# Performance work log

Hardware: AMD Instinct MI355X
Metric: run time of the kernel (lower is better)

Reference implementation:

```python
import jax, jax.numpy as jnp
import numpy as np

B, H, W, C = 16, 128, 128, 128
Wh = Ww = 8
SH = 4  # shift size
NH = 4  # heads
HD = C // NH
N = Wh * Ww
HID = 4 * C
EPS = 1e-3  # keras LayerNormalization default epsilon
SCALE = HD ** -0.5


def _rel_pos_index():
    coords = np.stack(np.meshgrid(np.arange(Wh), np.arange(Ww), indexing='ij'))  # (2,Wh,Ww)
    flat = coords.reshape(2, -1)
    rel = flat[:, :, None] - flat[:, None, :]  # (2,N,N)
    rel = rel.transpose(1, 2, 0) + np.array([Wh - 1, Ww - 1])
    rel = rel * np.array([2 * Ww - 1, 1])
    return rel.sum(-1).astype(np.int32)  # (N,N)


def _attn_mask():
    img = np.zeros((1, H, W, 1))
    h_sl = (slice(0, H - Wh), slice(H - Wh, H - SH), slice(H - SH, H))
    w_sl = (slice(0, W - Ww), slice(W - Ww, W - SH), slice(W - SH, W))
    cnt = 0
    for hs in h_sl:
        for ws in w_sl:
            img[:, hs, ws, :] = cnt
            cnt += 1
    mw = img.reshape(1, H // Wh, Wh, W // Ww, Ww, 1).transpose(0, 1, 3, 2, 4, 5).reshape(-1, N)
    am = mw[:, None, :] - mw[:, :, None]
    return np.where(am != 0, -100.0, 0.0).astype(np.float32)  # (nW,N,N)


def setup_inputs() -> dict:
    key = jax.random.key(0)
    ks = jax.random.split(key, 12)
    s = 0.02
    return {
        'x': jax.random.normal(ks[0], (B, H * W, C), jnp.float32),
        'w_qkv': jax.random.normal(ks[1], (C, 3 * C), jnp.float32) * s,
        'b_qkv': jnp.zeros((3 * C,), jnp.float32),
        'bias_table': jax.random.normal(ks[2], ((2 * Wh - 1) * (2 * Ww - 1), NH), jnp.float32) * s,
        'w_proj': jax.random.normal(ks[3], (C, C), jnp.float32) * s,
        'b_proj': jnp.zeros((C,), jnp.float32),
        'g1': jnp.ones((C,), jnp.float32),
        'be1': jnp.zeros((C,), jnp.float32),
        'w_fc1': jax.random.normal(ks[4], (C, HID), jnp.float32) * s,
        'b_fc1': jnp.zeros((HID,), jnp.float32),
        'w_fc2': jax.random.normal(ks[5], (HID, C), jnp.float32) * s,
        'b_fc2': jnp.zeros((C,), jnp.float32),
        'g2': jnp.ones((C,), jnp.float32),
        'be2': jnp.zeros((C,), jnp.float32),
        'rel_index': jnp.asarray(_rel_pos_index()),
        'attn_mask': jnp.asarray(_attn_mask()),
    }


def _ln(x, g, b):
    m = jnp.mean(x, -1, keepdims=True)
    v = jnp.mean(jnp.square(x - m), -1, keepdims=True)
    return (x - m) * jax.lax.rsqrt(v + EPS) * g + b


def _block(x, w_qkv, b_qkv, bias_table, w_proj, b_proj, g1, be1,
           w_fc1, b_fc1, w_fc2, b_fc2, g2, be2, rel_index, attn_mask):
    xi = x.reshape(B, H, W, C)
    xs = jnp.roll(xi, (-SH, -SH), axis=(1, 2))
    # window partition -> (B*nW, N, C)
    xw = xs.reshape(B, H // Wh, Wh, W // Ww, Ww, C).transpose(0, 1, 3, 2, 4, 5).reshape(-1, N, C)
    qkv = (xw @ w_qkv + b_qkv).reshape(-1, N, 3, NH, HD).transpose(2, 0, 3, 1, 4)
    q, k, v = qkv[0] * SCALE, qkv[1], qkv[2]
    attn = jnp.einsum('bhnd,bhmd->bhnm', q, k)  # (B*nW, NH, N, N)
    rpb = bias_table[rel_index.reshape(-1)].reshape(N, N, NH).transpose(2, 0, 1)
    attn = attn + rpb[None]
    nW = attn_mask.shape[0]
    attn = attn.reshape(-1, nW, NH, N, N) + attn_mask[None, :, None]
    attn = jax.nn.softmax(attn.reshape(-1, NH, N, N), axis=-1)
    out = jnp.einsum('bhnm,bhmd->bhnd', attn, v).transpose(0, 2, 1, 3).reshape(-1, N, C)
    out = out @ w_proj + b_proj
    # window reverse + unshift
    out = out.reshape(B, H // Wh, W // Ww, Wh, Ww, C).transpose(0, 1, 3, 2, 4, 5).reshape(B, H, W, C)
    out = jnp.roll(out, (SH, SH), axis=(1, 2)).reshape(B, H * W, C)
    # NOTE: this module applies norm AFTER the sublayers (post-norm residual)
    x = x + _ln(out, g1, be1)
    h = jax.nn.gelu(x @ w_fc1 + b_fc1, approximate=False) @ w_fc2 + b_fc2
    x = x + _ln(h, g2, be2)
    return x


def reference(x, w_qkv, b_qkv, bias_table, w_proj, b_proj, g1, be1,
              w_fc1, b_fc1, w_fc2, b_fc2, g2, be2, rel_index, attn_mask):
    return _block(x, w_qkv, b_qkv, bias_table, w_proj, b_proj, g1, be1,
                  w_fc1, b_fc1, w_fc2, b_fc2, g2, be2, rel_index, attn_mask)
```

## Files before the change

kernel.cpp:

```cpp
#include <hip/hip_runtime.h>
#include <hip/hip_bf16.h>
#include <math.h>

typedef unsigned short u16;
typedef unsigned int   u32;

typedef __bf16 bf16x8 __attribute__((ext_vector_type(8)));
typedef float  f32x4  __attribute__((ext_vector_type(4)));
#define MFMA_B16 __builtin_amdgcn_mfma_f32_16x16x32_bf16

__device__ __forceinline__ u16 f2b(float f) {
    union { __bf16 h; u16 u; } v; v.h = (__bf16)f; return v.u;
}
__device__ __forceinline__ u32 pk2(float a, float b) {
    union { __bf16 h[2]; u32 u; } v;
    v.h[0] = (__bf16)a; v.h[1] = (__bf16)b; return v.u;
}
__device__ __forceinline__ bf16x8 pk8(float4 f0, float4 f1) {
    bf16x8 r;
    r[0] = (__bf16)f0.x; r[1] = (__bf16)f0.y; r[2] = (__bf16)f0.z; r[3] = (__bf16)f0.w;
    r[4] = (__bf16)f1.x; r[5] = (__bf16)f1.y; r[6] = (__bf16)f1.z; r[7] = (__bf16)f1.w;
    return r;
}

__device__ __forceinline__ float gelu_fast(float v) {
    const float z = v * (1.5957691f + 0.07135486f * v * v);
    return v * __builtin_amdgcn_rcpf(1.0f + __expf(-z));
}

__device__ __forceinline__ int qk_idx(int row, int d) {
    return row * 32 + (d ^ (((row >> 1) & 3) << 3));
}
__device__ __forceinline__ int p_idx(int row, int col) {
    return row * 64 + (col ^ ((row & 7) << 3));
}

#define SCALE_ 0.17677669529663687f
#define EPS_   1e-3f


__global__ __launch_bounds__(256) void swin_prep(
    const float* __restrict__ w_qkv, const float* __restrict__ w_proj,
    const float* __restrict__ w_fc1, const float* __restrict__ w_fc2,
    const float* __restrict__ bias_table, const int* __restrict__ rel_index,
    const float* __restrict__ attn_mask,
    u16* __restrict__ wqkvT, u16* __restrict__ wprojT,
    u16* __restrict__ w1T, u16* __restrict__ w2T, float* __restrict__ rpbm)
{
    const int idx = blockIdx.x * 256 + threadIdx.x;
    if (idx < 49152) {
        const int o = idx >> 7, c = idx & 127;
        wqkvT[idx] = f2b(w_qkv[c * 384 + o]);
    } else if (idx < 65536) {
        const int i2 = idx - 49152;
        const int o = i2 >> 7, c = i2 & 127;
        wprojT[i2] = f2b(w_proj[c * 128 + o]);
    } else if (idx < 131072) {
        const int i2 = idx - 65536;
        const int o = i2 >> 7, c = i2 & 127;
        w1T[i2] = f2b(w_fc1[c * 512 + o]);
    } else if (idx < 196608) {
        const int i2 = idx - 131072;
        const int o = i2 >> 9, u = i2 & 511;
        w2T[i2] = f2b(w_fc2[u * 128 + o]);
    } else if (idx < 262144) {
        const int i2 = idx - 196608;
        const int cls = i2 >> 14, rem = i2 & 16383;
        const int h = rem >> 12, ij = rem & 4095;
        const int widx = ((cls & 2) ? 240 : 0) + ((cls & 1) ? 15 : 0);
        rpbm[i2] = bias_table[rel_index[ij] * 4 + h] + attn_mask[widx * 4096 + ij];
    }
}

#define VA_OFF  16384
#define AO_OFF  0
#define X2F_OFF 4352

__global__ __launch_bounds__(256, 3) void swin_attn_mfma(
    const float* __restrict__ x, const u16* __restrict__ wqkvT, const float* __restrict__ b_qkv,
    const u16* __restrict__ wprojT, const float* __restrict__ b_proj,
    const float* __restrict__ g1, const float* __restrict__ be1,
    const float* __restrict__ rpbm, float* __restrict__ x1out)
{
    __shared__ __align__(16) u16 sm[25600];
    const int tid  = threadIdx.x;
    const int w    = tid >> 6;
    const int lane = tid & 63;
    const int l15  = lane & 15;
    const int quad = lane >> 4;
    const int win  = blockIdx.x;
    const int b = win >> 8, wr = (win >> 4) & 15, wc = win & 15;

    size_t rowb[4];
    #pragma unroll
    for (int mi = 0; mi < 4; mi++) {
        const int t  = mi * 16 + l15;
        const int hh = (wr * 8 + (t >> 3) + 4) & 127;
        const int ww = (wc * 8 + (t & 7) + 4) & 127;
        rowb[mi] = ((size_t)((b * 128 + hh) * 128 + ww)) * 128;
    }

    {
        f32x4 acc[6][4];
        #pragma unroll
        for (int n = 0; n < 6; n++) {
            const float bq = b_qkv[(n >> 1) * 128 + w * 32 + (n & 1) * 16 + l15];
            #pragma unroll
            for (int mi = 0; mi < 4; mi++) acc[n][mi] = (f32x4){bq, bq, bq, bq};
        }
        #pragma unroll
        for (int ks = 0; ks < 4; ks++) {
            bf16x8 a[4], bb[6];
            #pragma unroll
            for (int mi = 0; mi < 4; mi++) {
                const float4 f0 = *(const float4*)(x + rowb[mi] + ks * 32 + quad * 8);
                const float4 f1 = *(const float4*)(x + rowb[mi] + ks * 32 + quad * 8 + 4);
                a[mi] = pk8(f0, f1);
            }
            #pragma unroll
            for (int n = 0; n < 6; n++)
                bb[n] = *(const bf16x8*)(wqkvT
                    + (size_t)((n >> 1) * 128 + w * 32 + (n & 1) * 16 + l15) * 128 + ks * 32 + quad * 8);
            #pragma unroll
            for (int n = 0; n < 6; n++)
                #pragma unroll
                for (int mi = 0; mi < 4; mi++)
                    acc[n][mi] = MFMA_B16(a[mi], bb[n], acc[n][mi], 0, 0, 0);
        }
        #pragma unroll
        for (int n = 0; n < 6; n++) {
            const int s = n >> 1, d = (n & 1) * 16 + l15;
            #pragma unroll
            for (int mi = 0; mi < 4; mi++) {
                if (s < 2) {
                    const int base = w * 4096 + s * 2048;
                    const float sc = s ? 1.0f : SCALE_;
                    #pragma unroll
                    for (int r = 0; r < 4; r++) {
                        const int row = mi * 16 + quad * 4 + r;
                        sm[base + qk_idx(row, d)] = f2b(acc[n][mi][r] * sc);
                    }
                } else {
                    const int t0 = mi * 16 + quad * 4;
                    const u32 w0 = pk2(acc[n][mi][0], acc[n][mi][1]);
                    const u32 w1 = pk2(acc[n][mi][2], acc[n][mi][3]);
                    *(uint2*)(sm + VA_OFF + w * 2304 + d * 72 + t0) = make_uint2(w0, w1);
                }
            }
        }
    }

    float sinv[4][4];
    {
        const float* rb = rpbm + (size_t)((((wr == 15) ? 2 : 0) | ((wc == 15) ? 1 : 0)) * 4 + w) * 4096;
        f32x4 S[4][4];
        #pragma unroll
        for (int mi = 0; mi < 4; mi++)
            #pragma unroll
            for (int ni = 0; ni < 4; ni++)
                #pragma unroll
                for (int r = 0; r < 4; r++)
                    S[mi][ni][r] = rb[(mi * 16 + quad * 4 + r) * 64 + ni * 16 + l15];
        bf16x8 aq[4], bk[4];
        #pragma unroll
        for (int mi = 0; mi < 4; mi++)
            aq[mi] = *(const bf16x8*)(sm + w * 4096 + qk_idx(mi * 16 + l15, quad * 8));
        #pragma unroll
        for (int ni = 0; ni < 4; ni++)
            bk[ni] = *(const bf16x8*)(sm + w * 4096 + 2048 + qk_idx(ni * 16 + l15, quad * 8));
        #pragma unroll
        for (int mi = 0; mi < 4; mi++)
            #pragma unroll
            for (int ni = 0; ni < 4; ni++)
                S[mi][ni] = MFMA_B16(aq[mi], bk[ni], S[mi][ni], 0, 0, 0);
        #pragma unroll
        for (int mi = 0; mi < 4; mi++) {
            #pragma unroll
            for (int r = 0; r < 4; r++) {
                float m0 = fmaxf(fmaxf(S[mi][0][r], S[mi][1][r]), fmaxf(S[mi][2][r], S[mi][3][r]));
                m0 = fmaxf(m0, __shfl_xor(m0, 1));
                m0 = fmaxf(m0, __shfl_xor(m0, 2));
                m0 = fmaxf(m0, __shfl_xor(m0, 4));
                m0 = fmaxf(m0, __shfl_xor(m0, 8));
                float s0 = 0.0f;
                #pragma unroll
                for (int ni = 0; ni < 4; ni++) {
                    const float e = __expf(S[mi][ni][r] - m0);
                    S[mi][ni][r] = e;
                    s0 += e;
                }
                s0 += __shfl_xor(s0, 1);
                s0 += __shfl_xor(s0, 2);
                s0 += __shfl_xor(s0, 4);
                s0 += __shfl_xor(s0, 8);
                sinv[mi][r] = __builtin_amdgcn_rcpf(s0);
            }
        }

        #pragma unroll
        for (int mi = 0; mi < 4; mi++)
            #pragma unroll
            for (int ni = 0; ni < 4; ni++)
                #pragma unroll
                for (int r = 0; r < 4; r++)
                    sm[w * 4096 + p_idx(mi * 16 + quad * 4 + r, ni * 16 + l15)] = f2b(S[mi][ni][r]);

        f32x4 O[4][2];
        #pragma unroll
        for (int mi = 0; mi < 4; mi++)
            #pragma unroll
            for (int ni = 0; ni < 2; ni++) O[mi][ni] = (f32x4){0.f, 0.f, 0.f, 0.f};
        #pragma unroll
        for (int ks = 0; ks < 2; ks++) {
            bf16x8 ap[4], bv[2];
            #pragma unroll
            for (int mi = 0; mi < 4; mi++)
                ap[mi] = *(const bf16x8*)(sm + w * 4096 + p_idx(mi * 16 + l15, ks * 32 + quad * 8));
            #pragma unroll
            for (int ni = 0; ni < 2; ni++)
                bv[ni] = *(const bf16x8*)(sm + VA_OFF + w * 2304 + (ni * 16 + l15) * 72 + ks * 32 + quad * 8);
            #pragma unroll
            for (int mi = 0; mi < 4; mi++)
                #pragma unroll
                for (int ni = 0; ni < 2; ni++)
                    O[mi][ni] = MFMA_B16(ap[mi], bv[ni], O[mi][ni], 0, 0, 0);
        }
        __syncthreads();

        #pragma unroll
        for (int mi = 0; mi < 4; mi++)
            #pragma unroll
            for (int ni = 0; ni < 2; ni++)
                #pragma unroll
                for (int r = 0; r < 4; r++)
                    sm[AO_OFF + (mi * 16 + quad * 4 + r) * 136 + w * 32 + ni * 16 + l15]
                        = f2b(O[mi][ni][r] * sinv[mi][r]);
    }
    __syncthreads();

    float4 xres[8];
    size_t gout;
    {
        const int t = tid >> 2, part = tid & 3;
        const int hh = (wr * 8 + (t >> 3) + 4) & 127;
        const int ww = (wc * 8 + (t & 7) + 4) & 127;
        gout = ((size_t)((b * 128 + hh) * 128 + ww)) * 128 + part * 32;
        #pragma unroll
        for (int k = 0; k < 8; k++)
            xres[k] = *(const float4*)(x + gout + k * 4);
    }
    {
        f32x4 X2[4][2];
        #pragma unroll
        for (int ni = 0; ni < 2; ni++) {
            const float bp = b_proj[w * 32 + ni * 16 + l15];
            #pragma unroll
            for (int mi = 0; mi < 4; mi++) X2[mi][ni] = (f32x4){bp, bp, bp, bp};
        }
        #pragma unroll
        for (int ks = 0; ks < 4; ks++) {
            bf16x8 aa[4], bw[2];
            #pragma unroll
            for (int mi = 0; mi < 4; mi++)
                aa[mi] = *(const bf16x8*)(sm + AO_OFF + (mi * 16 + l15) * 136 + ks * 32 + quad * 8);
            #pragma unroll
            for (int ni = 0; ni < 2; ni++)
                bw[ni] = *(const bf16x8*)(wprojT + (size_t)(w * 32 + ni * 16 + l15) * 128 + ks * 32 + quad * 8);
            #pragma unroll
            for (int mi = 0; mi < 4; mi++)
                #pragma unroll
                for (int ni = 0; ni < 2; ni++)
                    X2[mi][ni] = MFMA_B16(aa[mi], bw[ni], X2[mi][ni], 0, 0, 0);
        }
        float* X2f = (float*)sm + X2F_OFF;
        #pragma unroll
        for (int mi = 0; mi < 4; mi++)
            #pragma unroll
            for (int ni = 0; ni < 2; ni++)
                #pragma unroll
                for (int r = 0; r < 4; r++)
                    X2f[(mi * 16 + quad * 4 + r) * 132 + w * 32 + ni * 16 + l15] = X2[mi][ni][r];
    }
    __syncthreads();

    {
        const int t = tid >> 2, part = tid & 3;
        const float* Xr = (const float*)sm + X2F_OFF + t * 132 + part * 32;
        float4 xr[8];
        float s1 = 0.f, s2 = 0.f;
        #pragma unroll
        for (int k = 0; k < 8; k++) {
            xr[k] = *(const float4*)(Xr + k * 4);
            s1 += xr[k].x + xr[k].y + xr[k].z + xr[k].w;
            s2 += xr[k].x * xr[k].x + xr[k].y * xr[k].y
                + xr[k].z * xr[k].z + xr[k].w * xr[k].w;
        }
        s1 += __shfl_xor(s1, 1); s1 += __shfl_xor(s1, 2);
        s2 += __shfl_xor(s2, 1); s2 += __shfl_xor(s2, 2);
        const float m  = s1 * 0.0078125f;
        const float vr = fmaxf(s2 * 0.0078125f - m * m, 0.f);
        const float rs = rsqrtf(vr + EPS_);
        #pragma unroll
        for (int k = 0; k < 8; k++) {
            const int c4 = k * 4;
            const float4 gv = *(const float4*)(g1 + part * 32 + c4);
            const float4 bv = *(const float4*)(be1 + part * 32 + c4);
            float4 o;
            o.x = xres[k].x + (xr[k].x - m) * rs * gv.x + bv.x;
            o.y = xres[k].y + (xr[k].y - m) * rs * gv.y + bv.y;
            o.z = xres[k].z + (xr[k].z - m) * rs * gv.z + bv.z;
            o.w = xres[k].w + (xr[k].w - m) * rs * gv.w + bv.w;
            *(float4*)(x1out + gout + c4) = o;
        }
    }
}

#define HB0_OFF 8704
#define X3F_OFF 4352

__global__ __launch_bounds__(256, 3) void swin_mlp_mfma(
    float* __restrict__ x1io, const u16* __restrict__ w1T, const float* __restrict__ b_fc1,
    const u16* __restrict__ w2T, const float* __restrict__ b_fc2,
    const float* __restrict__ g2, const float* __restrict__ be2)
{
    __shared__ __align__(16) u16 sm[26112];
    const int tid  = threadIdx.x;
    const int w    = tid >> 6;
    const int lane = tid & 63;
    const int l15  = lane & 15;
    const int quad = lane >> 4;
    const size_t base = (size_t)blockIdx.x * 8192;

    for (int e = tid * 8; e < 8192; e += 2048) {
        const int t = e >> 7, c = e & 127;
        const float4 f0 = *(const float4*)(x1io + base + e);
        const float4 f1 = *(const float4*)(x1io + base + e + 4);
        union { bf16x8 v; uint4 u; } cv; cv.v = pk8(f0, f1);
        *(uint4*)(sm + t * 136 + c) = cv.u;
    }
    __syncthreads();

    f32x4 acc2[2][4];
    #pragma unroll
    for (int ni = 0; ni < 2; ni++) {
        const float bb = b_fc2[w * 32 + ni * 16 + l15];
        #pragma unroll
        for (int mi = 0; mi < 4; mi++) acc2[ni][mi] = (f32x4){bb, bb, bb, bb};
    }

    for (int ch = 0; ch < 4; ch++) {
        u16* hb = sm + HB0_OFF + (ch & 1) * 8704;
        f32x4 a1[2][4];
        #pragma unroll
        for (int ni = 0; ni < 2; ni++) {
            const float bb = b_fc1[ch * 128 + (w * 2 + ni) * 16 + l15];
            #pragma unroll
            for (int mi = 0; mi < 4; mi++) a1[ni][mi] = (f32x4){bb, bb, bb, bb};
        }
        #pragma unroll
        for (int ks = 0; ks < 4; ks++) {
            bf16x8 af[4], bf[2];
            #pragma unroll
            for (int mi = 0; mi < 4; mi++)
                af[mi] = *(const bf16x8*)(sm + (mi * 16 + l15) * 136 + ks * 32 + quad * 8);
            #pragma unroll
            for (int ni = 0; ni < 2; ni++)
                bf[ni] = *(const bf16x8*)(w1T + (size_t)(ch * 128 + (w * 2 + ni) * 16 + l15) * 128 + ks * 32 + quad * 8);
            #pragma unroll
            for (int ni = 0; ni < 2; ni++)
                #pragma unroll
                for (int mi = 0; mi < 4; mi++)
                    a1[ni][mi] = MFMA_B16(af[mi], bf[ni], a1[ni][mi], 0, 0, 0);
        }
        #pragma unroll
        for (int ni = 0; ni < 2; ni++)
            #pragma unroll
            for (int mi = 0; mi < 4; mi++)
                #pragma unroll
                for (int r = 0; r < 4; r++) {
                    const float v = gelu_fast(a1[ni][mi][r]);
                    hb[(mi * 16 + quad * 4 + r) * 136 + (w * 2 + ni) * 16 + l15] = f2b(v);
                }
        __syncthreads();
        #pragma unroll
        for (int ks = 0; ks < 4; ks++) {
            bf16x8 ah[4], bh[2];
            #pragma unroll
            for (int mi = 0; mi < 4; mi++)
                ah[mi] = *(const bf16x8*)(hb + (mi * 16 + l15) * 136 + ks * 32 + quad * 8);
            #pragma unroll
            for (int ni = 0; ni < 2; ni++)
                bh[ni] = *(const bf16x8*)(w2T + (size_t)(w * 32 + ni * 16 + l15) * 512 + ch * 128 + ks * 32 + quad * 8);
            #pragma unroll
            for (int ni = 0; ni < 2; ni++)
                #pragma unroll
                for (int mi = 0; mi < 4; mi++)
                    acc2[ni][mi] = MFMA_B16(ah[mi], bh[ni], acc2[ni][mi], 0, 0, 0);
        }
    }
    __syncthreads();

    {
        float* X3 = (float*)sm + X3F_OFF;
        #pragma unroll
        for (int ni = 0; ni < 2; ni++)
            #pragma unroll
            for (int mi = 0; mi < 4; mi++)
                #pragma unroll
                for (int r = 0; r < 4; r++)
                    X3[(mi * 16 + quad * 4 + r) * 132 + w * 32 + ni * 16 + l15] = acc2[ni][mi][r];
    }
    __syncthreads();

    {
        const int t = tid >> 2, part = tid & 3;
        const float* Xr = (const float*)sm + X3F_OFF + t * 132 + part * 32;
        float4 xr[8];
        float s1 = 0.f, s2 = 0.f;
        #pragma unroll
        for (int k = 0; k < 8; k++) {
            xr[k] = *(const float4*)(Xr + k * 4);
            s1 += xr[k].x + xr[k].y + xr[k].z + xr[k].w;
            s2 += xr[k].x * xr[k].x + xr[k].y * xr[k].y
                + xr[k].z * xr[k].z + xr[k].w * xr[k].w;
        }
        s1 += __shfl_xor(s1, 1); s1 += __shfl_xor(s1, 2);
        s2 += __shfl_xor(s2, 1); s2 += __shfl_xor(s2, 2);
        const float m  = s1 * 0.0078125f;
        const float vr = fmaxf(s2 * 0.0078125f - m * m, 0.f);
        const float rs = rsqrtf(vr + EPS_);
        const size_t g = base + t * 128 + part * 32;
        #pragma unroll
        for (int k = 0; k < 8; k++) {
            const int c4 = k * 4;
            const float4 xv = *(const float4*)(x1io + g + c4);
            const float4 gv = *(const float4*)(g2 + part * 32 + c4);
            const float4 bv = *(const float4*)(be2 + part * 32 + c4);
            float4 o;
            o.x = xv.x + (xr[k].x - m) * rs * gv.x + bv.x;
            o.y = xv.y + (xr[k].y - m) * rs * gv.y + bv.y;
            o.z = xv.z + (xr[k].z - m) * rs * gv.z + bv.z;
            o.w = xv.w + (xr[k].w - m) * rs * gv.w + bv.w;
            *(float4*)(x1io + g + c4) = o;
        }
    }
}

extern "C" void kernel_launch(void* const* d_in, const int* in_sizes, int n_in,
                              void* d_out, int out_size, void* d_ws, size_t ws_size,
                              hipStream_t stream) {
    const float* x         = (const float*)d_in[0];
    const float* w_qkv     = (const float*)d_in[1];
    const float* b_qkv     = (const float*)d_in[2];
    const float* bias_tab  = (const float*)d_in[3];
    const float* w_proj    = (const float*)d_in[4];
    const float* b_proj    = (const float*)d_in[5];
    const float* g1        = (const float*)d_in[6];
    const float* be1       = (const float*)d_in[7];
    const float* w_fc1     = (const float*)d_in[8];
    const float* b_fc1     = (const float*)d_in[9];
    const float* w_fc2     = (const float*)d_in[10];
    const float* b_fc2     = (const float*)d_in[11];
    const float* g2        = (const float*)d_in[12];
    const float* be2       = (const float*)d_in[13];
    const int* rel_index   = (const int*)d_in[14];
    const float* attn_mask = (const float*)d_in[15];

    char* ws = (char*)d_ws;
    u16*   wqkvT  = (u16*)ws;
    u16*   wprojT = (u16*)(ws + 98304);
    u16*   w1T    = (u16*)(ws + 131072);
    u16*   w2T    = (u16*)(ws + 262144);
    float* rpbm   = (float*)(ws + 393216);

    float* x1 = (float*)d_out;

    swin_prep<<<1024, 256, 0, stream>>>(w_qkv, w_proj, w_fc1, w_fc2,
                                        bias_tab, rel_index, attn_mask,
                                        wqkvT, wprojT, w1T, w2T, rpbm);
    swin_attn_mfma<<<4096, 256, 0, stream>>>(x, wqkvT, b_qkv, wprojT, b_proj,
                                             g1, be1, rpbm, x1);
    swin_mlp_mfma<<<4096, 256, 0, stream>>>(x1, w1T, b_fc1, w2T, b_fc2, g2, be2);
}
```

Baseline: 625.3 us.

## Keep V in registers via shuffles and shrink attention LDS to raise occupancy

V is now computed first in its own MFMA pass and kept packed as bf16 in registers. Lanes exchange it with cross-lane shuffles to build the PV MFMA B operands, so V no longer needs its own LDS region. The projection output is staged in LDS as bf16 instead of fp32, which cuts shared memory from about 51KB to 35KB and lets launch bounds go from 3 to 4 blocks per CU. In exchange the kernel issues more shuffles, reloads x for a second QKV pass, keeps more registers live, and loses some precision on the pre-LayerNorm values.

```diff
diff --git a/kernel.cpp b/kernel.cpp
--- a/kernel.cpp
+++ b/kernel.cpp
@@ -21,6 +21,9 @@
     r[0] = (__bf16)f0.x; r[1] = (__bf16)f0.y; r[2] = (__bf16)f0.z; r[3] = (__bf16)f0.w;
     r[4] = (__bf16)f1.x; r[5] = (__bf16)f1.y; r[6] = (__bf16)f1.z; r[7] = (__bf16)f1.w;
     return r;
+}
+__device__ __forceinline__ float b2f(u16 u) {
+    union { u32 i; float f; } v; v.i = ((u32)u) << 16; return v.f;
 }
 
 __device__ __forceinline__ float gelu_fast(float v) {
@@ -72,17 +75,16 @@
     }
 }
 
-#define VA_OFF  16384
-#define AO_OFF  0
-#define X2F_OFF 4352
-
-__global__ __launch_bounds__(256, 3) void swin_attn_mfma(
+#define AO_OFF   0
+#define X2B_OFF  8704
+
+__global__ __launch_bounds__(256, 4) void swin_attn_mfma(
     const float* __restrict__ x, const u16* __restrict__ wqkvT, const float* __restrict__ b_qkv,
     const u16* __restrict__ wprojT, const float* __restrict__ b_proj,
     const float* __restrict__ g1, const float* __restrict__ be1,
     const float* __restrict__ rpbm, float* __restrict__ x1out)
 {
-    __shared__ __align__(16) u16 sm[25600];
+    __shared__ __align__(16) u16 sm[17408];
     const int tid  = threadIdx.x;
     const int w    = tid >> 6;
     const int lane = tid & 63;
@@ -100,17 +102,18 @@
         rowb[mi] = ((size_t)((b * 128 + hh) * 128 + ww)) * 128;
     }
 
-    {
-        f32x4 acc[6][4];
-        #pragma unroll
-        for (int n = 0; n < 6; n++) {
-            const float bq = b_qkv[(n >> 1) * 128 + w * 32 + (n & 1) * 16 + l15];
-            #pragma unroll
-            for (int mi = 0; mi < 4; mi++) acc[n][mi] = (f32x4){bq, bq, bq, bq};
+    u32 vpk[2][4][2];
+    {
+        f32x4 accv[2][4];
+        #pragma unroll
+        for (int ni = 0; ni < 2; ni++) {
+            const float bq = b_qkv[256 + w * 32 + ni * 16 + l15];
+            #pragma unroll
+            for (int mi = 0; mi < 4; mi++) accv[ni][mi] = (f32x4){bq, bq, bq, bq};
         }
         #pragma unroll
         for (int ks = 0; ks < 4; ks++) {
-            bf16x8 a[4], bb[6];
+            bf16x8 a[4], bb[2];
             #pragma unroll
             for (int mi = 0; mi < 4; mi++) {
                 const float4 f0 = *(const float4*)(x + rowb[mi] + ks * 32 + quad * 8);
@@ -118,35 +121,63 @@
                 a[mi] = pk8(f0, f1);
             }
             #pragma unroll
-            for (int n = 0; n < 6; n++)
+            for (int ni = 0; ni < 2; ni++)
+                bb[ni] = *(const bf16x8*)(wqkvT
+                    + (size_t)(256 + w * 32 + ni * 16 + l15) * 128 + ks * 32 + quad * 8);
+            #pragma unroll
+            for (int ni = 0; ni < 2; ni++)
+                #pragma unroll
+                for (int mi = 0; mi < 4; mi++)
+                    accv[ni][mi] = MFMA_B16(a[mi], bb[ni], accv[ni][mi], 0, 0, 0);
+        }
+        #pragma unroll
+        for (int ni = 0; ni < 2; ni++)
+            #pragma unroll
+            for (int mi = 0; mi < 4; mi++) {
+                vpk[ni][mi][0] = pk2(accv[ni][mi][0], accv[ni][mi][1]);
+                vpk[ni][mi][1] = pk2(accv[ni][mi][2], accv[ni][mi][3]);
+            }
+    }
+
+    {
+        f32x4 acc[4][4];
+        #pragma unroll
+        for (int n = 0; n < 4; n++) {
+            const float bq = b_qkv[(n >> 1) * 128 + w * 32 + (n & 1) * 16 + l15];
+            #pragma unroll
+            for (int mi = 0; mi < 4; mi++) acc[n][mi] = (f32x4){bq, bq, bq, bq};
+        }
+        #pragma unroll
+        for (int ks = 0; ks < 4; ks++) {
+            bf16x8 a[4], bb[4];
+            #pragma unroll
+            for (int mi = 0; mi < 4; mi++) {
+                const float4 f0 = *(const float4*)(x + rowb[mi] + ks * 32 + quad * 8);
+                const float4 f1 = *(const float4*)(x + rowb[mi] + ks * 32 + quad * 8 + 4);
+                a[mi] = pk8(f0, f1);
+            }
+            #pragma unroll
+            for (int n = 0; n < 4; n++)
                 bb[n] = *(const bf16x8*)(wqkvT
                     + (size_t)((n >> 1) * 128 + w * 32 + (n & 1) * 16 + l15) * 128 + ks * 32 + quad * 8);
             #pragma unroll
-            for (int n = 0; n < 6; n++)
+            for (int n = 0; n < 4; n++)
                 #pragma unroll
                 for (int mi = 0; mi < 4; mi++)
                     acc[n][mi] = MFMA_B16(a[mi], bb[n], acc[n][mi], 0, 0, 0);
         }
         #pragma unroll
-        for (int n = 0; n < 6; n++) {
+        for (int n = 0; n < 4; n++) {
             const int s = n >> 1, d = (n & 1) * 16 + l15;
-            #pragma unroll
-            for (int mi = 0; mi < 4; mi++) {
-                if (s < 2) {
-                    const int base = w * 4096 + s * 2048;
-                    const float sc = s ? 1.0f : SCALE_;
-                    #pragma unroll
-                    for (int r = 0; r < 4; r++) {
-                        const int row = mi * 16 + quad * 4 + r;
-                        sm[base + qk_idx(row, d)] = f2b(acc[n][mi][r] * sc);
-                    }
-                } else {
-                    const int t0 = mi * 16 + quad * 4;
-                    const u32 w0 = pk2(acc[n][mi][0], acc[n][mi][1]);
-                    const u32 w1 = pk2(acc[n][mi][2], acc[n][mi][3]);
-                    *(uint2*)(sm + VA_OFF + w * 2304 + d * 72 + t0) = make_uint2(w0, w1);
+            const int base = w * 4096 + s * 2048;
+            const float sc = s ? 1.0f : SCALE_;
+            #pragma unroll
+            for (int mi = 0; mi < 4; mi++)
+                #pragma unroll
+                for (int r = 0; r < 4; r++) {
+                    const int row = mi * 16 + quad * 4 + r;
+                    sm[base + qk_idx(row, d)] = f2b(acc[n][mi][r] * sc);
                 }
-            }
         }
     }
 
@@ -205,6 +236,10 @@
                 for (int r = 0; r < 4; r++)
                     sm[w * 4096 + p_idx(mi * 16 + quad * 4 + r, ni * 16 + l15)] = f2b(S[mi][ni][r]);
 
+        const int qs0 = ((lane & 16) << 1) | l15;
+        const int qs1 = qs0 + 16;
+        const bool hiPair = (lane & 32) != 0;
+
         f32x4 O[4][2];
         #pragma unroll
         for (int mi = 0; mi < 4; mi++)
@@ -217,8 +252,22 @@
             for (int mi = 0; mi < 4; mi++)
                 ap[mi] = *(const bf16x8*)(sm + w * 4096 + p_idx(mi * 16 + l15, ks * 32 + quad * 8));
             #pragma unroll
-            for (int ni = 0; ni < 2; ni++)
-                bv[ni] = *(const bf16x8*)(sm + VA_OFF + w * 2304 + (ni * 16 + l15) * 72 + ks * 32 + quad * 8);
+            for (int ni = 0; ni < 2; ni++) {
+                const u32 loA0 = __shfl(vpk[ni][2 * ks][0],     qs0);
+                const u32 loA1 = __shfl(vpk[ni][2 * ks][1],     qs0);
+                const u32 loB0 = __shfl(vpk[ni][2 * ks][0],     qs1);
+                const u32 loB1 = __shfl(vpk[ni][2 * ks][1],     qs1);
+                const u32 hiA0 = __shfl(vpk[ni][2 * ks + 1][0], qs0);
+                const u32 hiA1 = __shfl(vpk[ni][2 * ks + 1][1], qs0);
+                const u32 hiB0 = __shfl(vpk[ni][2 * ks + 1][0], qs1);
+                const u32 hiB1 = __shfl(vpk[ni][2 * ks + 1][1], qs1);
+                union { u32 u[4]; bf16x8 v; } cv;
+                cv.u[0] = hiPair ? hiA0 : loA0;
+                cv.u[1] = hiPair ? hiA1 : loA1;
+                cv.u[2] = hiPair ? hiB0 : loB0;
+                cv.u[3] = hiPair ? hiB1 : loB1;
+                bv[ni] = cv.v;
+            }
             #pragma unroll
             for (int mi = 0; mi < 4; mi++)
                 #pragma unroll
@@ -272,28 +321,31 @@
                 for (int ni = 0; ni < 2; ni++)
                     X2[mi][ni] = MFMA_B16(aa[mi], bw[ni], X2[mi][ni], 0, 0, 0);
         }
-        float* X2f = (float*)sm + X2F_OFF;
         #pragma unroll
         for (int mi = 0; mi < 4; mi++)
             #pragma unroll
             for (int ni = 0; ni < 2; ni++)
                 #pragma unroll
                 for (int r = 0; r < 4; r++)
-                    X2f[(mi * 16 + quad * 4 + r) * 132 + w * 32 + ni * 16 + l15] = X2[mi][ni][r];
+                    sm[X2B_OFF + (mi * 16 + quad * 4 + r) * 136 + w * 32 + ni * 16 + l15]
+                        = f2b(X2[mi][ni][r]);
     }
     __syncthreads();
 
     {
         const int t = tid >> 2, part = tid & 3;
-        const float* Xr = (const float*)sm + X2F_OFF + t * 132 + part * 32;
-        float4 xr[8];
+        const u16* Xr = sm + X2B_OFF + t * 136 + part * 32;
+        float xv[32];
         float s1 = 0.f, s2 = 0.f;
         #pragma unroll
-        for (int k = 0; k < 8; k++) {
-            xr[k] = *(const float4*)(Xr + k * 4);
-            s1 += xr[k].x + xr[k].y + xr[k].z + xr[k].w;
-            s2 += xr[k].x * xr[k].x + xr[k].y * xr[k].y
-                + xr[k].z * xr[k].z + xr[k].w * xr[k].w;
+        for (int k = 0; k < 4; k++) {
+            const bf16x8 v8 = *(const bf16x8*)(Xr + k * 8);
+            #pragma unroll
+            for (int e = 0; e < 8; e++) {
+                const float v = (float)v8[e];
+                xv[k * 8 + e] = v;
+                s1 += v; s2 += v * v;
+            }
         }
         s1 += __shfl_xor(s1, 1); s1 += __shfl_xor(s1, 2);
         s2 += __shfl_xor(s2, 1); s2 += __shfl_xor(s2, 2);
@@ -306,10 +358,10 @@
             const float4 gv = *(const float4*)(g1 + part * 32 + c4);
             const float4 bv = *(const float4*)(be1 + part * 32 + c4);
             float4 o;
-            o.x = xres[k].x + (xr[k].x - m) * rs * gv.x + bv.x;
-            o.y = xres[k].y + (xr[k].y - m) * rs * gv.y + bv.y;
-            o.z = xres[k].z + (xr[k].z - m) * rs * gv.z + bv.z;
-            o.w = xres[k].w + (xr[k].w - m) * rs * gv.w + bv.w;
+            o.x = xres[k].x + (xv[c4 + 0] - m) * rs * gv.x + bv.x;
+            o.y = xres[k].y + (xv[c4 + 1] - m) * rs * gv.y + bv.y;
+            o.z = xres[k].z + (xv[c4 + 2] - m) * rs * gv.z + bv.z;
+            o.w = xres[k].w + (xv[c4 + 3] - m) * rs * gv.w + bv.w;
             *(float4*)(x1out + gout + c4) = o;
         }
     }
```

After: 798.6 us. +27.7%, slower.
